# Optimization experiments

Hardware: AMD Instinct MI355X
Metric: run time of the kernel (lower is better)

Reference implementation:

```python
import jax, jax.numpy as jnp
import numpy as np

N = 100000      # nodes == in_ch (transductive: x = arange(N))
E = 3200000     # nonzeros of sparse hypergraph adjacency G (COO)
D = 128         # i_emb
DROPOUT = 0.1


def setup_inputs() -> dict:
    key = jax.random.key(0)
    k1, k2, k3, k4, k5 = jax.random.split(key, 5)
    x = jnp.arange(N, dtype=jnp.int64) if jax.config.jax_enable_x64 else jnp.arange(N, dtype=jnp.int32)
    row = jax.random.randint(k1, (E,), 0, N, dtype=jnp.int32)
    col = jax.random.randint(k2, (E,), 0, N, dtype=jnp.int32)
    vals = jax.random.uniform(k3, (E,), dtype=jnp.float32)
    # xavier-uniform embedding: bound = sqrt(6/(N+D))
    eb = float(np.sqrt(6.0 / (N + D)))
    embed_w = jax.random.uniform(k4, (N, D), jnp.float32, -eb, eb)
    fb = float(np.sqrt(6.0 / (D + D)))
    fc_w = jax.random.uniform(k5, (D, D), jnp.float32, -fb, fb)
    fc_b = jnp.zeros((D,), jnp.float32)
    return {"x": x, "row": row, "col": col, "vals": vals,
            "embed_w": embed_w, "fc_w": fc_w, "fc_b": fc_b}


def reference(x, row, col, vals, embed_w, fc_w, fc_b):
    e = embed_w[x]                                   # [N, D] embedding lookup
    # SpMM: out[i] = sum_{nz} vals * e[col]  scattered to row
    agg = jax.ops.segment_sum(vals[:, None] * e[col], row, num_segments=e.shape[0])
    m1 = agg + e                                     # residual
    keep = 1.0 - DROPOUT                             # F.dropout (training=True default)
    mask = jax.random.bernoulli(jax.random.key(42), keep, m1.shape)
    m1 = jnp.where(mask, m1 / keep, 0.0)
    x1 = jax.nn.leaky_relu(m1 @ fc_w.T + fc_b, negative_slope=0.2)
    return jnp.concatenate((e, x1), axis=1)          # [N, 2D]
```

## Files before the change

### kernel.cpp

```cpp
#include <hip/hip_runtime.h>


#define NN 100000
#define DD 128
#define EE 3200000
#define SCAN_B 256
#define NBLK ((NN + SCAN_B - 1) / SCAN_B)

__device__ __forceinline__ unsigned rotl32(unsigned v, int s) {
    return (v << s) | (v >> (32 - s));
}

__device__ __forceinline__ bool keep_elem(unsigned idx) {
    unsigned x0 = 0u, x1 = idx;
    const unsigned k0 = 0u, k1 = 42u;
    const unsigned k2 = 0x1BD11BDAu ^ k0 ^ k1;
    x0 += k0; x1 += k1;
#define TFROUND(s) x0 += x1; x1 = rotl32(x1, s); x1 ^= x0;
    TFROUND(13) TFROUND(15) TFROUND(26) TFROUND(6)
    x0 += k1; x1 += k2 + 1u;
    TFROUND(17) TFROUND(29) TFROUND(16) TFROUND(24)
    x0 += k2; x1 += k0 + 2u;
    TFROUND(13) TFROUND(15) TFROUND(26) TFROUND(6)
    x0 += k0; x1 += k1 + 3u;
    TFROUND(17) TFROUND(29) TFROUND(16) TFROUND(24)
    x0 += k1; x1 += k2 + 4u;
    TFROUND(13) TFROUND(15) TFROUND(26) TFROUND(6)
    x0 += k2; x1 += k0 + 5u;
#undef TFROUND
    unsigned bits = x0 ^ x1;
    float u = __uint_as_float((bits >> 9) | 0x3f800000u) - 1.0f;
    return u < 0.9f;
}

__global__ __launch_bounds__(256) void setup_kernel(const float4* __restrict__ emb4,
                                                    uint2* __restrict__ ebf2,
                                                    int4* __restrict__ counts4) {
    int i = blockIdx.x * 256 + threadIdx.x;
    float4 v = emb4[i];
    unsigned a = __float_as_uint(v.x), b = __float_as_uint(v.y);
    unsigned c = __float_as_uint(v.z), d = __float_as_uint(v.w);
    a = (a + 0x7fffu + ((a >> 16) & 1u)) >> 16;
    b = (b + 0x7fffu + ((b >> 16) & 1u)) >> 16;
    c = (c + 0x7fffu + ((c >> 16) & 1u)) >> 16;
    d = (d + 0x7fffu + ((d >> 16) & 1u)) >> 16;
    uint2 o;
    o.x = a | (b << 16);
    o.y = c | (d << 16);
    ebf2[i] = o;
    if (i < NN / 4) counts4[i] = make_int4(0, 0, 0, 0);
}

__global__ __launch_bounds__(256) void hist_kernel(const int4* __restrict__ row4,
                                                   int* __restrict__ counts,
                                                   int4* __restrict__ rank4) {
    int i = blockIdx.x * 256 + threadIdx.x;
    int4 r = row4[i];
    int4 k;
    k.x = atomicAdd(&counts[r.x], 1);
    k.y = atomicAdd(&counts[r.y], 1);
    k.z = atomicAdd(&counts[r.z], 1);
    k.w = atomicAdd(&counts[r.w], 1);
    rank4[i] = k;
}

__global__ __launch_bounds__(SCAN_B) void scan1_kernel(const int* __restrict__ counts,
                                                       int* __restrict__ rowptr,
                                                       int* __restrict__ bsums) {
    __shared__ int s[SCAN_B];
    int t = threadIdx.x;
    int i = blockIdx.x * SCAN_B + t;
    int v = (i < NN) ? counts[i] : 0;
    s[t] = v;
    __syncthreads();
    for (int d = 1; d < SCAN_B; d <<= 1) {
        int a = (t >= d) ? s[t - d] : 0;
        __syncthreads();
        s[t] += a;
        __syncthreads();
    }
    if (i < NN) rowptr[i + 1] = s[t];
    if (t == SCAN_B - 1) bsums[blockIdx.x] = s[t];
}

__global__ __launch_bounds__(512) void scan2_kernel(int* __restrict__ bsums) {
    __shared__ int s[512];
    int t = threadIdx.x;
    int v = (t < NBLK) ? bsums[t] : 0;
    s[t] = v;
    __syncthreads();
    for (int d = 1; d < 512; d <<= 1) {
        int a = (t >= d) ? s[t - d] : 0;
        __syncthreads();
        s[t] += a;
        __syncthreads();
    }
    if (t < NBLK) bsums[t] = s[t] - v;
}

__global__ __launch_bounds__(SCAN_B) void scan3_kernel(int* __restrict__ rowptr,
                                                       const int* __restrict__ bsums) {
    int i = blockIdx.x * SCAN_B + threadIdx.x;
    if (i < NN) rowptr[i + 1] += bsums[i >> 8];
    if (i == 0) rowptr[0] = 0;
}

__device__ __forceinline__ unsigned pack_entry(int xc, float v) {
    unsigned pb = __float_as_uint(v) + 0x10000u;
    return (pb & 0xFFFE0000u) | (unsigned)xc;
}

__global__ __launch_bounds__(256) void fill_kernel(const int* __restrict__ x,
                                                   const int4* __restrict__ row4,
                                                   const int4* __restrict__ col4,
                                                   const float4* __restrict__ vals4,
                                                   const int4* __restrict__ rank4,
                                                   const int* __restrict__ rowptr,
                                                   unsigned* __restrict__ csr) {
    int i = blockIdx.x * 256 + threadIdx.x;
    int4 r = row4[i];
    int4 c = col4[i];
    float4 v = vals4[i];
    int4 k = rank4[i];
    csr[rowptr[r.x] + k.x] = pack_entry(x[c.x], v.x);
    csr[rowptr[r.y] + k.y] = pack_entry(x[c.y], v.y);
    csr[rowptr[r.z] + k.z] = pack_entry(x[c.z], v.z);
    csr[rowptr[r.w] + k.w] = pack_entry(x[c.w], v.w);
}

__global__ __launch_bounds__(256) void gather_kernel(const int* __restrict__ x,
                                                     const int* __restrict__ rowptr,
                                                     const unsigned* __restrict__ csr,
                                                     const unsigned* __restrict__ ebf,
                                                     const float2* __restrict__ emb2,
                                                     float2* __restrict__ out2) {
    int wave = threadIdx.x >> 6;
    int lane = threadIdx.x & 63;
    int n = blockIdx.x * 4 + wave;
    int s = rowptr[n], e = rowptr[n + 1];
    float ax = 0.f, ay = 0.f;
    int j = s;
    for (; j + 4 <= e; j += 4) {
        unsigned p0 = csr[j], p1 = csr[j + 1], p2 = csr[j + 2], p3 = csr[j + 3];
        unsigned b0 = ebf[(long)(p0 & 0x1FFFFu) * 64 + lane];
        unsigned b1 = ebf[(long)(p1 & 0x1FFFFu) * 64 + lane];
        unsigned b2 = ebf[(long)(p2 & 0x1FFFFu) * 64 + lane];
        unsigned b3 = ebf[(long)(p3 & 0x1FFFFu) * 64 + lane];
        float v0 = __uint_as_float(p0 & 0xFFFE0000u);
        float v1 = __uint_as_float(p1 & 0xFFFE0000u);
        float v2 = __uint_as_float(p2 & 0xFFFE0000u);
        float v3 = __uint_as_float(p3 & 0xFFFE0000u);
        ax += v0 * __uint_as_float(b0 << 16) + v1 * __uint_as_float(b1 << 16)
            + v2 * __uint_as_float(b2 << 16) + v3 * __uint_as_float(b3 << 16);
        ay += v0 * __uint_as_float(b0 & 0xffff0000u) + v1 * __uint_as_float(b1 & 0xffff0000u)
            + v2 * __uint_as_float(b2 & 0xffff0000u) + v3 * __uint_as_float(b3 & 0xffff0000u);
    }
    for (; j < e; ++j) {
        unsigned p = csr[j];
        unsigned b = ebf[(long)(p & 0x1FFFFu) * 64 + lane];
        float v = __uint_as_float(p & 0xFFFE0000u);
        ax += v * __uint_as_float(b << 16);
        ay += v * __uint_as_float(b & 0xffff0000u);
    }
    float2 es = emb2[(long)x[n] * 64 + lane];
    out2[(long)n * 128 + lane] = es;
    float2 m1;
    m1.x = ax + es.x;
    m1.y = ay + es.y;
    out2[(long)n * 128 + 64 + lane] = m1;
}

__global__ __launch_bounds__(256) void fc_kernel(float* __restrict__ out,
                                                 const float* __restrict__ fc_w,
                                                 const float* __restrict__ fc_b) {
    __shared__ float wt[128][132];
    __shared__ float ms[32][128];
    int tid = threadIdx.x;
    int row0 = blockIdx.x * 32;

    for (int i = tid; i < 128 * 128; i += 256) {
        int j = i >> 7, k = i & 127;
        wt[k][j] = fc_w[i];
    }
    for (int i = tid; i < 32 * 32; i += 256) {
        int r = i >> 5, q = i & 31;
        long n = row0 + r;
        float4 v = *(const float4*)(out + n * 256 + 128 + q * 4);
        unsigned base = (unsigned)n * 128u + (unsigned)(q * 4);
        float* vp = reinterpret_cast<float*>(&v);
#pragma unroll
        for (int c = 0; c < 4; ++c)
            vp[c] = keep_elem(base + c) ? vp[c] * (1.0f / 0.9f) : 0.0f;
        *(float4*)(&ms[r][q * 4]) = v;
    }
    __syncthreads();

    int rg = tid >> 5;
    int cg = tid & 31;
    float acc[4][4] = {{0.f}};
    for (int k = 0; k < 128; ++k) {
        float4 w4 = *(const float4*)(&wt[k][cg * 4]);
#pragma unroll
        for (int r = 0; r < 4; ++r) {
            float m = ms[rg * 4 + r][k];
            acc[r][0] += m * w4.x;
            acc[r][1] += m * w4.y;
            acc[r][2] += m * w4.z;
            acc[r][3] += m * w4.w;
        }
    }

    float4 b4 = *(const float4*)(fc_b + cg * 4);
#pragma unroll
    for (int r = 0; r < 4; ++r) {
        long n = row0 + rg * 4 + r;
        float4 o;
        o.x = acc[r][0] + b4.x;
        o.y = acc[r][1] + b4.y;
        o.z = acc[r][2] + b4.z;
        o.w = acc[r][3] + b4.w;
        o.x = o.x >= 0.f ? o.x : 0.2f * o.x;
        o.y = o.y >= 0.f ? o.y : 0.2f * o.y;
        o.z = o.z >= 0.f ? o.z : 0.2f * o.z;
        o.w = o.w >= 0.f ? o.w : 0.2f * o.w;
        *(float4*)(out + n * 256 + 128 + cg * 4) = o;
    }
}

__global__ __launch_bounds__(256) void init_kernel(const int* __restrict__ x,
                                                   const float4* __restrict__ emb4,
                                                   float4* __restrict__ out4) {
    int i = blockIdx.x * 256 + threadIdx.x;
    int n = i >> 5;
    int q = i & 31;
    if (n >= NN) return;
    float4 v = emb4[(long)x[n] * 32 + q];
    out4[(long)n * 64 + q] = v;
    out4[(long)n * 64 + 32 + q] = v;
}

#define EDGES_PER_GROUP 8
__global__ __launch_bounds__(256) void scatter_kernel(const int* __restrict__ x,
                                                      const int* __restrict__ row,
                                                      const int* __restrict__ col,
                                                      const float* __restrict__ vals,
                                                      const float4* __restrict__ emb4,
                                                      float* __restrict__ out) {
    long gid = (long)blockIdx.x * 256 + threadIdx.x;
    long group = gid >> 5;
    int lane = (int)(gid & 31);
    long e0 = group * EDGES_PER_GROUP;
#pragma unroll
    for (int k = 0; k < EDGES_PER_GROUP; ++k) {
        long e = e0 + k;
        if (e >= EE) break;
        int r = row[e];
        int c = col[e];
        float v = vals[e];
        float4 ev = emb4[(long)x[c] * 32 + lane];
        float* dst = out + (long)r * 256 + 128 + lane * 4;
        atomicAdd(dst + 0, v * ev.x);
        atomicAdd(dst + 1, v * ev.y);
        atomicAdd(dst + 2, v * ev.z);
        atomicAdd(dst + 3, v * ev.w);
    }
}

extern "C" void kernel_launch(void* const* d_in, const int* in_sizes, int n_in,
                              void* d_out, int out_size, void* d_ws, size_t ws_size,
                              hipStream_t stream) {
    const int*   x    = (const int*)d_in[0];
    const int*   row  = (const int*)d_in[1];
    const int*   col  = (const int*)d_in[2];
    const float* vals = (const float*)d_in[3];
    const float* emb  = (const float*)d_in[4];
    const float* fc_w = (const float*)d_in[5];
    const float* fc_b = (const float*)d_in[6];
    float* out = (float*)d_out;

    size_t off = 0;
    char* ws = (char*)d_ws;
    int* counts = (int*)(ws + off); off += (((size_t)NN * 4) + 255) & ~(size_t)255;
    int* rowptr = (int*)(ws + off); off += (((size_t)(NN + 1) * 4) + 255) & ~(size_t)255;
    int* bsums  = (int*)(ws + off); off += 4096;
    unsigned* csr = (unsigned*)(ws + off); off += (size_t)EE * 4;
    int* rank   = (int*)(ws + off); off += (size_t)EE * 4;
    unsigned* ebf = (unsigned*)(ws + off); off += (size_t)NN * DD * 2;
    size_t need = off;

    if (ws_size >= need) {
        setup_kernel<<<(int)(((long)NN * DD / 4 + 255) / 256), 256, 0, stream>>>(
            (const float4*)emb, (uint2*)ebf, (int4*)counts);
        hist_kernel<<<EE / 4 / 256, 256, 0, stream>>>((const int4*)row, counts, (int4*)rank);
        scan1_kernel<<<NBLK, SCAN_B, 0, stream>>>(counts, rowptr, bsums);
        scan2_kernel<<<1, 512, 0, stream>>>(bsums);
        scan3_kernel<<<NBLK, SCAN_B, 0, stream>>>(rowptr, bsums);
        fill_kernel<<<EE / 4 / 256, 256, 0, stream>>>(x, (const int4*)row, (const int4*)col,
                                                      (const float4*)vals, (const int4*)rank,
                                                      rowptr, csr);
        gather_kernel<<<NN / 4, 256, 0, stream>>>(x, rowptr, csr, ebf,
                                                  (const float2*)emb, (float2*)out);
    } else {
        init_kernel<<<(NN * 32 + 255) / 256, 256, 0, stream>>>(x, (const float4*)emb, (float4*)out);
        int scatter_blocks = (int)(((long)EE / EDGES_PER_GROUP) * 32 / 256);
        scatter_kernel<<<scatter_blocks, 256, 0, stream>>>(x, row, col, vals,
                                                           (const float4*)emb, out);
    }

    fc_kernel<<<NN / 32, 256, 0, stream>>>(out, fc_w, fc_b);
}
```

Before: 658.9 us.

## Fuse dropout into gather and add higher-reuse fc kernel for CSR path

Applies the dropout mask and scaling in the gather epilogue, and adds a new fc3 kernel that tiles 64 rows per block. Its weights are staged in 32-wide k-chunks with a transposed activation tile. Presumably the old fc kernel did the dropout itself and loaded the full 128x128 weight per 32 rows. The new kernel amortizes weight loads over more rows and aims for 3 blocks per SM, at the cost of more registers per thread. The fallback path keeps the old fc_kernel.

```diff
diff --git a/kernel.cpp b/kernel.cpp
--- a/kernel.cpp
+++ b/kernel.cpp
@@ -167,7 +167,129 @@
     float2 m1;
     m1.x = ax + es.x;
     m1.y = ay + es.y;
+    unsigned base = (unsigned)n * 128u + 2u * (unsigned)lane;
+    m1.x = keep_elem(base) ? m1.x * (1.0f / 0.9f) : 0.0f;
+    m1.y = keep_elem(base + 1u) ? m1.y * (1.0f / 0.9f) : 0.0f;
     out2[(long)n * 128 + 64 + lane] = m1;
+}
+
+__global__ __launch_bounds__(256, 3) void fc3_kernel(float* __restrict__ out,
+                                                     const float* __restrict__ fc_w,
+                                                     const float* __restrict__ fc_b) {
+    __shared__ float ms_t[128][66];
+    __shared__ float wc[32][132];
+    int tid = threadIdx.x;
+    int row0 = blockIdx.x * 64;
+    const float4* fcw4 = (const float4*)fc_w;
+    const float4* out4c = (const float4*)out;
+
+    for (int chunk = tid; chunk < 64 * 32; chunk += 256) {
+        int nl = chunk >> 5;
+        int q = chunk & 31;
+        int n = row0 + nl;
+        float4 v = (n < NN) ? out4c[(long)n * 64 + 32 + q]
+                            : make_float4(0.f, 0.f, 0.f, 0.f);
+        ms_t[q * 4 + 0][nl] = v.x;
+        ms_t[q * 4 + 1][nl] = v.y;
+        ms_t[q * 4 + 2][nl] = v.z;
+        ms_t[q * 4 + 3][nl] = v.w;
+    }
+
+    int cg = tid & 31;
+    int rg = tid >> 5;
+    float acc[8][4];
+#pragma unroll
+    for (int r = 0; r < 8; ++r)
+#pragma unroll
+        for (int c = 0; c < 4; ++c) acc[r][c] = 0.f;
+
+    for (int ch = 0; ch < 4; ++ch) {
+        __syncthreads();
+        for (int chunk = tid; chunk < 128 * 8; chunk += 256) {
+            int jj = chunk >> 3;
+            int kq = chunk & 7;
+            float4 v = fcw4[jj * 32 + ch * 8 + kq];
+            wc[kq * 4 + 0][jj] = v.x;
+            wc[kq * 4 + 1][jj] = v.y;
+            wc[kq * 4 + 2][jj] = v.z;
+            wc[kq * 4 + 3][jj] = v.w;
+        }
+        __syncthreads();
+        int kbase = ch * 32;
+#pragma unroll
+        for (int kk = 0; kk < 32; ++kk) {
+            float4 w4 = *(const float4*)(&wc[kk][cg * 4]);
+            int k = kbase + kk;
+            float2 m01 = *(const float2*)(&ms_t[k][rg * 8 + 0]);
+            float2 m23 = *(const float2*)(&ms_t[k][rg * 8 + 2]);
+            float2 m45 = *(const float2*)(&ms_t[k][rg * 8 + 4]);
+            float2 m67 = *(const float2*)(&ms_t[k][rg * 8 + 6]);
+            float m[8] = {m01.x, m01.y, m23.x, m23.y, m45.x, m45.y, m67.x, m67.y};
+#pragma unroll
+            for (int r = 0; r < 8; ++r) {
+                acc[r][0] += m[r] * w4.x;
+                acc[r][1] += m[r] * w4.y;
+                acc[r][2] += m[r] * w4.z;
+                acc[r][3] += m[r] * w4.w;
+            }
+        }
+    }
+
+    float4 b4 = *(const float4*)(fc_b + cg * 4);
+#pragma unroll
+    for (int r = 0; r < 8; ++r) {
+        int n = row0 + rg * 8 + r;
+        if (n >= NN) break;
+        float4 o;
+        o.x = acc[r][0] + b4.x;
+        o.y = acc[r][1] + b4.y;
+        o.z = acc[r][2] + b4.z;
+        o.w = acc[r][3] + b4.w;
+        o.x = o.x >= 0.f ? o.x : 0.2f * o.x;
+        o.y = o.y >= 0.f ? o.y : 0.2f * o.y;
+        o.z = o.z >= 0.f ? o.z : 0.2f * o.z;
+        o.w = o.w >= 0.f ? o.w : 0.2f * o.w;
+        *(float4*)(out + (long)n * 256 + 128 + cg * 4) = o;
+    }
+}
+
+__global__ __launch_bounds__(256) void init_kernel(const int* __restrict__ x,
+                                                   const float4* __restrict__ emb4,
+                                                   float4* __restrict__ out4) {
+    int i = blockIdx.x * 256 + threadIdx.x;
+    int n = i >> 5;
+    int q = i & 31;
+    if (n >= NN) return;
+    float4 v = emb4[(long)x[n] * 32 + q];
+    out4[(long)n * 64 + q] = v;
+    out4[(long)n * 64 + 32 + q] = v;
+}
+
+#define EDGES_PER_GROUP 8
+__global__ __launch_bounds__(256) void scatter_kernel(const int* __restrict__ x,
+                                                      const int* __restrict__ row,
+                                                      const int* __restrict__ col,
+                                                      const float* __restrict__ vals,
+                                                      const float4* __restrict__ emb4,
+                                                      float* __restrict__ out) {
+    long gid = (long)blockIdx.x * 256 + threadIdx.x;
+    long group = gid >> 5;
+    int lane = (int)(gid & 31);
+    long e0 = group * EDGES_PER_GROUP;
+#pragma unroll
+    for (int k = 0; k < EDGES_PER_GROUP; ++k) {
+        long e = e0 + k;
+        if (e >= EE) break;
+        int r = row[e];
+        int c = col[e];
+        float v = vals[e];
+        float4 ev = emb4[(long)x[c] * 32 + lane];
+        float* dst = out + (long)r * 256 + 128 + lane * 4;
+        atomicAdd(dst + 0, v * ev.x);
+        atomicAdd(dst + 1, v * ev.y);
+        atomicAdd(dst + 2, v * ev.z);
+        atomicAdd(dst + 3, v * ev.w);
+    }
 }
 
 __global__ __launch_bounds__(256) void fc_kernel(float* __restrict__ out,
@@ -227,45 +349,6 @@
     }
 }
 
-__global__ __launch_bounds__(256) void init_kernel(const int* __restrict__ x,
-                                                   const float4* __restrict__ emb4,
-                                                   float4* __restrict__ out4) {
-    int i = blockIdx.x * 256 + threadIdx.x;
-    int n = i >> 5;
-    int q = i & 31;
-    if (n >= NN) return;
-    float4 v = emb4[(long)x[n] * 32 + q];
-    out4[(long)n * 64 + q] = v;
-    out4[(long)n * 64 + 32 + q] = v;
-}
-
-#define EDGES_PER_GROUP 8
-__global__ __launch_bounds__(256) void scatter_kernel(const int* __restrict__ x,
-                                                      const int* __restrict__ row,
-                                                      const int* __restrict__ col,
-                                                      const float* __restrict__ vals,
-                                                      const float4* __restrict__ emb4,
-                                                      float* __restrict__ out) {
-    long gid = (long)blockIdx.x * 256 + threadIdx.x;
-    long group = gid >> 5;
-    int lane = (int)(gid & 31);
-    long e0 = group * EDGES_PER_GROUP;
-#pragma unroll
-    for (int k = 0; k < EDGES_PER_GROUP; ++k) {
-        long e = e0 + k;
-        if (e >= EE) break;
-        int r = row[e];
-        int c = col[e];
-        float v = vals[e];
-        float4 ev = emb4[(long)x[c] * 32 + lane];
-        float* dst = out + (long)r * 256 + 128 + lane * 4;
-        atomicAdd(dst + 0, v * ev.x);
-        atomicAdd(dst + 1, v * ev.y);
-        atomicAdd(dst + 2, v * ev.z);
-        atomicAdd(dst + 3, v * ev.w);
-    }
-}
-
 extern "C" void kernel_launch(void* const* d_in, const int* in_sizes, int n_in,
                               void* d_out, int out_size, void* d_ws, size_t ws_size,
                               hipStream_t stream) {
@@ -300,12 +383,12 @@
                                                       rowptr, csr);
         gather_kernel<<<NN / 4, 256, 0, stream>>>(x, rowptr, csr, ebf,
                                                   (const float2*)emb, (float2*)out);
+        fc3_kernel<<<(NN + 63) / 64, 256, 0, stream>>>(out, fc_w, fc_b);
     } else {
         init_kernel<<<(NN * 32 + 255) / 256, 256, 0, stream>>>(x, (const float4*)emb, (float4*)out);
         int scatter_blocks = (int)(((long)EE / EDGES_PER_GROUP) * 32 / 256);
         scatter_kernel<<<scatter_blocks, 256, 0, stream>>>(x, row, col, vals,
                                                            (const float4*)emb, out);
-    }
-
-    fc_kernel<<<NN / 32, 256, 0, stream>>>(out, fc_w, fc_b);
-}
+        fc_kernel<<<NN / 32, 256, 0, stream>>>(out, fc_w, fc_b);
+    }
+}
```

After: 590.8 us. -10.3%, faster.
